# Kernel optimization log

Hardware: AMD Instinct MI355X
Metric: run time of the kernel (lower is better)

The kernel has to match this reference:

```python
import jax, jax.numpy as jnp
import numpy as np

EMBED = 1024
HEADS = 16
HEAD_DIM = EMBED // HEADS
FF = 4096
EPS = 1e-5


def layer_norm(x, g, b):
    mu = jnp.mean(x, axis=-1, keepdims=True)
    var = jnp.mean(jnp.square(x - mu), axis=-1, keepdims=True)
    return (x - mu) * jax.lax.rsqrt(var + EPS) * g + b


def setup_inputs() -> dict:
    key = jax.random.key(0)
    ks = jax.random.split(key, 16)
    s = 0.02
    x = jax.random.normal(ks[0], (4, 2048, EMBED), dtype=jnp.float32)
    d = {
        "x": x,
        "Wq": jax.random.normal(ks[1], (EMBED, EMBED), jnp.float32) * s,
        "bq": jnp.zeros((EMBED,), jnp.float32),
        "Wk": jax.random.normal(ks[2], (EMBED, EMBED), jnp.float32) * s,
        "bk": jnp.zeros((EMBED,), jnp.float32),
        "Wv": jax.random.normal(ks[3], (EMBED, EMBED), jnp.float32) * s,
        "bv": jnp.zeros((EMBED,), jnp.float32),
        "Wo": jax.random.normal(ks[4], (EMBED, EMBED), jnp.float32) * s,
        "bo": jnp.zeros((EMBED,), jnp.float32),
        "W1": jax.random.normal(ks[5], (EMBED, FF), jnp.float32) * s,
        "b1": jnp.zeros((FF,), jnp.float32),
        "W2": jax.random.normal(ks[6], (FF, EMBED), jnp.float32) * s,
        "b2": jnp.zeros((EMBED,), jnp.float32),
        "ln1_g": jnp.ones((EMBED,), jnp.float32),
        "ln1_b": jnp.zeros((EMBED,), jnp.float32),
        "ln2_g": jnp.ones((EMBED,), jnp.float32),
        "ln2_b": jnp.zeros((EMBED,), jnp.float32),
    }
    return d


def reference(x, Wq, bq, Wk, bk, Wv, bv, Wo, bo, W1, b1, W2, b2, ln1_g, ln1_b, ln2_g, ln2_b):
    B, S, E = x.shape
    scale = np.sqrt(HEAD_DIM).astype(np.float32)
    # project and split heads: (B, H, S, Dh)
    def heads(t):
        return t.reshape(B, S, HEADS, HEAD_DIM).transpose(0, 2, 1, 3)
    Q = heads(x @ Wq + bq)
    K = heads(x @ Wk + bk)
    V = heads(x @ Wv + bv)
    scores = jnp.einsum("bhqd,bhkd->bhqk", Q, K) / scale
    attn = jax.nn.softmax(scores, axis=-1)
    ctx = jnp.einsum("bhqk,bhkd->bhqd", attn, V)
    ctx = ctx.transpose(0, 2, 1, 3).reshape(B, S, E)
    attn_out = ctx @ Wo + bo
    x = layer_norm(x + attn_out, ln1_g, ln1_b)
    ff = jax.nn.relu(x @ W1 + b1) @ W2 + b2
    x = layer_norm(x + ff, ln2_g, ln2_b)
    return x
```

## Files before the change

kernel.cpp:

```cpp
#include <hip/hip_runtime.h>
#include <stdint.h>

typedef uint16_t u16;
typedef __bf16 bf16x8 __attribute__((ext_vector_type(8)));
typedef float f32x4 __attribute__((ext_vector_type(4)));

__device__ __forceinline__ float bf2f(u16 u) {
  union { uint32_t i; float f; } v; v.i = ((uint32_t)u) << 16; return v.f;
}
__device__ __forceinline__ u16 f2bf(float f) {
  union { float f; uint32_t i; } v; v.f = f;
  uint32_t r = v.i + 0x7fffu + ((v.i >> 16) & 1u);
  return (u16)(r >> 16);
}
__device__ __forceinline__ uint32_t pack2(float a, float b) {
  return (uint32_t)f2bf(a) | ((uint32_t)f2bf(b) << 16);
}
__device__ __forceinline__ void gll16(const u16* g, u16* l) {
  __builtin_amdgcn_global_load_lds((const __attribute__((address_space(1))) void*)g,
                                   (__attribute__((address_space(3))) void*)l, 16, 0, 0);
}

__global__ __launch_bounds__(256) void f32_to_bf16(
    const float* __restrict__ in, u16* __restrict__ out)
{
  int idx = blockIdx.x * 256 + threadIdx.x;
  float4 v = *(const float4*)(in + (size_t)idx * 4);
  uint2 o;
  o.x = pack2(v.x, v.y);
  o.y = pack2(v.z, v.w);
  *(uint2*)(out + (size_t)idx * 4) = o;
}

__global__ __launch_bounds__(256) void concat_bias(
    const float* __restrict__ a, const float* __restrict__ b,
    const float* __restrict__ c, float* __restrict__ o)
{
  int i = blockIdx.x * 256 + threadIdx.x;
  float v = (i < 1024) ? a[i] : ((i < 2048) ? b[i - 1024] : c[i - 2048]);
  o[i] = v;
}

__global__ __launch_bounds__(256) void transpose_f2b(
    const float* __restrict__ in, u16* __restrict__ out, int R, int C, int ldo)
{
  __shared__ u16 tile[32][33];
  int c0 = blockIdx.x * 32, r0 = blockIdx.y * 32;
  int x = threadIdx.x, y = threadIdx.y;
#pragma unroll
  for (int i = 0; i < 32; i += 8)
    tile[y + i][x] = f2bf(in[(size_t)(r0 + y + i) * C + (c0 + x)]);
  __syncthreads();
#pragma unroll
  for (int i = 0; i < 32; i += 8)
    out[(size_t)(c0 + y + i) * ldo + (r0 + x)] = tile[x][y + i];
}

__global__ __launch_bounds__(256) void transpose_v(
    const u16* __restrict__ src, u16* __restrict__ dst)
{
  __shared__ u16 tile[64][72];
  int kc = blockIdx.x;
  int bh = blockIdx.y;
  int b = bh >> 4, h = bh & 15;
  int t = threadIdx.x;
  int r = t >> 3;
  int c0 = (t & 7) * 8;
  const u16* s0 = src + ((size_t)(b * 2048 + kc * 64 + r) * 3072) + h * 64 + c0;
#pragma unroll
  for (int hh = 0; hh < 2; hh++)
    *(uint4*)(&tile[r + hh * 32][c0]) = *(const uint4*)(s0 + (size_t)hh * 32 * 3072);
  __syncthreads();
#pragma unroll
  for (int hh = 0; hh < 2; hh++) {
    int d = r + hh * 32;
    u16 vals[8];
#pragma unroll
    for (int p = 0; p < 8; p++) {
      int pos = c0 + p;
      int key = ((pos & 3) << 4) | ((pos >> 2) & 15);
      vals[p] = tile[key][d];
    }
    *(uint4*)(dst + ((size_t)bh * 64 + d) * 2048 + (size_t)kc * 64 + c0) = *(uint4*)vals;
  }
}

#define BM 128
#define BN 128
#define BK 32

__global__ __launch_bounds__(256, 2) void gemm_bt(
    const u16* __restrict__ A, const u16* __restrict__ BT,
    const float* __restrict__ bias, u16* __restrict__ C,
    int N, int K, int lda, int ldb, int ldc, int relu, int addC)
{
  __shared__ __align__(16) u16 As[BM][BK];
  __shared__ __align__(16) u16 Bs[BN][BK];
  int tid = threadIdx.x;
  int m0 = blockIdx.y * BM, n0 = blockIdx.x * BN;
  int wave = tid >> 6, lane = tid & 63;
  int quad = lane >> 4, tr = lane & 15;
  int wm = (wave >> 1) * 64, wn = (wave & 1) * 64;

  f32x4 zero = {0.f, 0.f, 0.f, 0.f};
  f32x4 acc[4][4];
#pragma unroll
  for (int i = 0; i < 4; i++)
#pragma unroll
    for (int j = 0; j < 4; j++) acc[i][j] = zero;

  int r_s = tid >> 2;
  int c_s = (tid & 3) * 8;
  const u16* Aptr = A + (size_t)(m0 + r_s) * lda + c_s;
  const u16* Bptr = BT + (size_t)(n0 + r_s) * ldb + c_s;
  u16* lA0 = &As[r_s][c_s];
  u16* lA1 = &As[r_s + 64][c_s];
  u16* lB0 = &Bs[r_s][c_s];
  u16* lB1 = &Bs[r_s + 64][c_s];

  for (int k0 = 0; k0 < K; k0 += BK) {
    gll16(Aptr + k0, lA0);
    gll16(Aptr + (size_t)64 * lda + k0, lA1);
    gll16(Bptr + k0, lB0);
    gll16(Bptr + (size_t)64 * ldb + k0, lB1);
    __syncthreads();
    bf16x8 af[4], bfr[4];
#pragma unroll
    for (int i = 0; i < 4; i++) af[i]  = *(const bf16x8*)(&As[wm + i*16 + tr][quad*8]);
#pragma unroll
    for (int j = 0; j < 4; j++) bfr[j] = *(const bf16x8*)(&Bs[wn + j*16 + tr][quad*8]);
#pragma unroll
    for (int i = 0; i < 4; i++)
#pragma unroll
      for (int j = 0; j < 4; j++)
        acc[i][j] = __builtin_amdgcn_mfma_f32_16x16x32_bf16(af[i], bfr[j], acc[i][j], 0, 0, 0);
    __syncthreads();
  }

#pragma unroll
  for (int j = 0; j < 4; j++) {
    int n = n0 + wn + j*16 + tr;
    float bv = bias ? bias[n] : 0.f;
#pragma unroll
    for (int i = 0; i < 4; i++) {
      int mrow = m0 + wm + i*16 + quad*4;
#pragma unroll
      for (int r = 0; r < 4; r++) {
        size_t idx = (size_t)(mrow + r) * ldc + n;
        float v = acc[i][j][r] + bv;
        if (addC) v += bf2f(C[idx]);
        if (relu) v = v > 0.f ? v : 0.f;
        C[idx] = f2bf(v);
      }
    }
  }
}

__global__ __launch_bounds__(512, 4) void flash_attn(
    const u16* __restrict__ Qb, const u16* __restrict__ Kb,
    const u16* __restrict__ Vtg, u16* __restrict__ Ob, int ldqkv, int ldo)
{
  __shared__ __align__(16) u16 Ks[64][72];
  __shared__ __align__(16) u16 Vt[64][72];
  __shared__ __align__(16) u16 Ps[8][32][72];

  const int S = 2048;
  int tid = threadIdx.x;
  int wv = tid >> 6, lane = tid & 63;
  int quad = lane >> 4, tr = lane & 15;
  int bh = blockIdx.y;
  int b = bh >> 4, h = bh & 15;
  int q0 = blockIdx.x * 256;
  int wq = wv * 32;
  size_t rowbase = (size_t)b * S;
  int colbase = h * 64;

  bf16x8 qf[2][2];
#pragma unroll
  for (int i = 0; i < 2; i++)
#pragma unroll
    for (int ks = 0; ks < 2; ks++)
      qf[i][ks] = *(const bf16x8*)(Qb + (rowbase + q0 + wq + i*16 + tr) * ldqkv
                                   + colbase + ks*32 + quad*8);

  f32x4 zero = {0.f, 0.f, 0.f, 0.f};
  f32x4 o[2][4];
  float lsum[2][4];
#pragma unroll
  for (int i = 0; i < 2; i++)
#pragma unroll
    for (int r = 0; r < 4; r++) lsum[i][r] = 0.f;
#pragma unroll
  for (int i = 0; i < 2; i++)
#pragma unroll
    for (int j = 0; j < 4; j++) o[i][j] = zero;

  const float sc = 0.125f;

  int srow = tid >> 3;
  int scol = (tid & 7) * 8;
  const u16* vt_base = Vtg + ((size_t)bh * 64 + srow) * 2048 + scol;

  for (int kv0 = 0; kv0 < S; kv0 += 64) {
    *(uint4*)(&Ks[srow][scol]) =
        *(const uint4*)(Kb + (rowbase + kv0 + srow) * ldqkv + colbase + scol);
    *(uint4*)(&Vt[srow][scol]) = *(const uint4*)(vt_base + kv0);
    __syncthreads();

    f32x4 s[2][4];
#pragma unroll
    for (int i = 0; i < 2; i++)
#pragma unroll
      for (int j = 0; j < 4; j++) s[i][j] = zero;
#pragma unroll
    for (int ks = 0; ks < 2; ks++) {
      bf16x8 kf[4];
#pragma unroll
      for (int j = 0; j < 4; j++)
        kf[j] = *(const bf16x8*)(&Ks[j*16 + tr][ks*32 + quad*8]);
#pragma unroll
      for (int i = 0; i < 2; i++)
#pragma unroll
        for (int j = 0; j < 4; j++)
          s[i][j] = __builtin_amdgcn_mfma_f32_16x16x32_bf16(qf[i][ks], kf[j], s[i][j], 0, 0, 0);
    }

#pragma unroll
    for (int i = 0; i < 2; i++) {
#pragma unroll
      for (int r = 0; r < 4; r++) {
        float p0 = __expf(s[i][0][r] * sc);
        float p1 = __expf(s[i][1][r] * sc);
        float p2 = __expf(s[i][2][r] * sc);
        float p3 = __expf(s[i][3][r] * sc);
        lsum[i][r] += (p0 + p1) + (p2 + p3);
        uint2 w;
        w.x = (__float_as_uint(p0) >> 16) | (__float_as_uint(p1) & 0xffff0000u);
        w.y = (__float_as_uint(p2) >> 16) | (__float_as_uint(p3) & 0xffff0000u);
        *(uint2*)(&Ps[wv][i*16 + quad*4 + r][tr*4]) = w;
      }
    }

#pragma unroll
    for (int ks = 0; ks < 2; ks++) {
      bf16x8 pf[2];
#pragma unroll
      for (int i = 0; i < 2; i++)
        pf[i] = *(const bf16x8*)(&Ps[wv][i*16 + tr][ks*32 + quad*8]);
#pragma unroll
      for (int jd = 0; jd < 4; jd++) {
        bf16x8 vf = *(const bf16x8*)(&Vt[jd*16 + tr][ks*32 + quad*8]);
#pragma unroll
        for (int i = 0; i < 2; i++)
          o[i][jd] = __builtin_amdgcn_mfma_f32_16x16x32_bf16(pf[i], vf, o[i][jd], 0, 0, 0);
      }
    }
    __syncthreads();
  }

#pragma unroll
  for (int i = 0; i < 2; i++) {
#pragma unroll
    for (int r = 0; r < 4; r++) {
      float l = lsum[i][r];
      l += __shfl_xor(l, 1, 64);
      l += __shfl_xor(l, 2, 64);
      l += __shfl_xor(l, 4, 64);
      l += __shfl_xor(l, 8, 64);
      float inv = 1.f / l;
      size_t qrow = rowbase + q0 + wq + i*16 + quad*4 + r;
#pragma unroll
      for (int jd = 0; jd < 4; jd++)
        Ob[qrow * ldo + colbase + jd*16 + tr] = f2bf(o[i][jd][r] * inv);
    }
  }
}

__global__ __launch_bounds__(256) void add_ln_a(
    const float* __restrict__ X, const u16* __restrict__ Rr,
    const float* __restrict__ G, const float* __restrict__ Bb,
    u16* __restrict__ Y)
{
  int row = blockIdx.x;
  int tid = threadIdx.x;
  __shared__ float sbuf[4], qbuf[4];
  float4 xv = *(const float4*)(X + (size_t)row * 1024 + tid * 4);
  uint2 ru = *(const uint2*)(Rr + (size_t)row * 1024 + tid * 4);
  const u16* rs = (const u16*)&ru;
  const float* xs = (const float*)&xv;
  float v[4];
  float s = 0.f, q = 0.f;
#pragma unroll
  for (int e = 0; e < 4; e++) {
    float a = xs[e] + bf2f(rs[e]);
    v[e] = a; s += a; q += a * a;
  }
#pragma unroll
  for (int off = 1; off < 64; off <<= 1) {
    s += __shfl_xor(s, off, 64);
    q += __shfl_xor(q, off, 64);
  }
  if ((tid & 63) == 0) { sbuf[tid >> 6] = s; qbuf[tid >> 6] = q; }
  __syncthreads();
  s = sbuf[0] + sbuf[1] + sbuf[2] + sbuf[3];
  q = qbuf[0] + qbuf[1] + qbuf[2] + qbuf[3];
  float mu  = s * (1.f / 1024.f);
  float var = q * (1.f / 1024.f) - mu * mu;
  float inv = rsqrtf(var + 1e-5f);
#pragma unroll
  for (int e = 0; e < 4; e++) {
    int col = tid * 4 + e;
    float yv = (v[e] - mu) * inv * G[col] + Bb[col];
    Y[(size_t)row * 1024 + col] = f2bf(yv);
  }
}

__global__ __launch_bounds__(256) void add_ln_b(
    const u16* __restrict__ X, const u16* __restrict__ Rr,
    const float* __restrict__ G, const float* __restrict__ Bb,
    float* __restrict__ Y)
{
  int row = blockIdx.x;
  int tid = threadIdx.x;
  __shared__ float sbuf[4], qbuf[4];
  uint2 xu = *(const uint2*)(X  + (size_t)row * 1024 + tid * 4);
  uint2 ru = *(const uint2*)(Rr + (size_t)row * 1024 + tid * 4);
  const u16* xs = (const u16*)&xu;
  const u16* rs = (const u16*)&ru;
  float v[4];
  float s = 0.f, q = 0.f;
#pragma unroll
  for (int e = 0; e < 4; e++) {
    float a = bf2f(xs[e]) + bf2f(rs[e]);
    v[e] = a; s += a; q += a * a;
  }
#pragma unroll
  for (int off = 1; off < 64; off <<= 1) {
    s += __shfl_xor(s, off, 64);
    q += __shfl_xor(q, off, 64);
  }
  if ((tid & 63) == 0) { sbuf[tid >> 6] = s; qbuf[tid >> 6] = q; }
  __syncthreads();
  s = sbuf[0] + sbuf[1] + sbuf[2] + sbuf[3];
  q = qbuf[0] + qbuf[1] + qbuf[2] + qbuf[3];
  float mu  = s * (1.f / 1024.f);
  float var = q * (1.f / 1024.f) - mu * mu;
  float inv = rsqrtf(var + 1e-5f);
  float4 yv;
  float* yp = (float*)&yv;
#pragma unroll
  for (int e = 0; e < 4; e++) {
    int col = tid * 4 + e;
    yp[e] = (v[e] - mu) * inv * G[col] + Bb[col];
  }
  *(float4*)(Y + (size_t)row * 1024 + tid * 4) = yv;
}

extern "C" void kernel_launch(void* const* d_in, const int* in_sizes, int n_in,
                              void* d_out, int out_size, void* d_ws, size_t ws_size,
                              hipStream_t stream) {
  const float* x   = (const float*)d_in[0];
  const float* Wq  = (const float*)d_in[1];
  const float* bq  = (const float*)d_in[2];
  const float* Wk  = (const float*)d_in[3];
  const float* bk  = (const float*)d_in[4];
  const float* Wv  = (const float*)d_in[5];
  const float* bv  = (const float*)d_in[6];
  const float* Wo  = (const float*)d_in[7];
  const float* bo  = (const float*)d_in[8];
  const float* W1  = (const float*)d_in[9];
  const float* b1  = (const float*)d_in[10];
  const float* W2  = (const float*)d_in[11];
  const float* b2  = (const float*)d_in[12];
  const float* g1  = (const float*)d_in[13];
  const float* be1 = (const float*)d_in[14];
  const float* g2  = (const float*)d_in[15];
  const float* be2 = (const float*)d_in[16];
  float* out = (float*)d_out;
  u16* ws  = (u16*)d_ws;

  const int Nrow = 8192, E = 1024, FFd = 4096;
  const size_t M1 = 1048576;
  u16* xb     = ws;
  u16* WqkvT  = ws + 8  * M1;
  u16* WoT    = ws + 11 * M1;
  u16* W1T    = ws + 12 * M1;
  u16* W2T    = ws + 16 * M1;
  u16* QKV    = ws + 20 * M1;
  u16* Vtg    = ws;
  u16* X1     = ws;
  u16* F2     = ws + 20 * M1;
  float* bqkv = (float*)d_out;
  u16*  AO    = (u16*)d_out;
  u16*  Hc    = (u16*)d_out;

  dim3 tb(256);
  dim3 tt(32, 8);
  f32_to_bf16<<<dim3(8192), tb, 0, stream>>>(x, xb);
  transpose_f2b<<<dim3(E/32,  E/32),  tt, 0, stream>>>(Wq, WqkvT,        E,   E,   E);
  transpose_f2b<<<dim3(E/32,  E/32),  tt, 0, stream>>>(Wk, WqkvT + 1*M1, E,   E,   E);
  transpose_f2b<<<dim3(E/32,  E/32),  tt, 0, stream>>>(Wv, WqkvT + 2*M1, E,   E,   E);
  transpose_f2b<<<dim3(E/32,  E/32),  tt, 0, stream>>>(Wo, WoT,          E,   E,   E);
  transpose_f2b<<<dim3(FFd/32,E/32),  tt, 0, stream>>>(W1, W1T,          E,   FFd, E);
  transpose_f2b<<<dim3(E/32,  FFd/32),tt, 0, stream>>>(W2, W2T,          FFd, E,   FFd);
  concat_bias<<<dim3(12), tb, 0, stream>>>(bq, bk, bv, bqkv);

  gemm_bt<<<dim3(24, Nrow/BM), tb, 0, stream>>>(xb, WqkvT, bqkv, QKV,
                                                3072, E, E, E, 3072, 0, 0);
  transpose_v<<<dim3(32, 64), tb, 0, stream>>>(QKV + 2048, Vtg);
  flash_attn<<<dim3(8, 64), dim3(512), 0, stream>>>(QKV, QKV + 1024, Vtg,
                                                    QKV + 2048, 3072, 3072);
  gemm_bt<<<dim3(8, Nrow/BM), tb, 0, stream>>>(QKV + 2048, WoT, bo, AO,
                                               E, E, 3072, E, E, 0, 0);
  add_ln_a<<<dim3(Nrow), tb, 0, stream>>>(x, AO, g1, be1, X1);

  for (int c = 0; c < 2; c++) {
    gemm_bt<<<dim3(16, Nrow/BM), tb, 0, stream>>>(
        X1, W1T + (size_t)c * 2048 * E, b1 + c * 2048, Hc,
        2048, E, E, E, 2048, 1, 0);
    gemm_bt<<<dim3(8, Nrow/BM), tb, 0, stream>>>(
        Hc, W2T + (size_t)c * 2048, (c == 0 ? b2 : (const float*)nullptr), F2,
        E, 2048, 2048, FFd, E, 0, (c == 0 ? 0 : 1));
  }

  add_ln_b<<<dim3(Nrow), tb, 0, stream>>>(X1, F2, g2, be2, out);
}
```

Measured before the change: 593.5 us.

## Double GEMM K-tile, add XOR-swizzled LDS layout, use direct-to-LDS loads in attention

```diff
diff --git a/kernel.cpp b/kernel.cpp
--- a/kernel.cpp
+++ b/kernel.cpp
@@ -87,7 +87,7 @@
 
 #define BM 128
 #define BN 128
-#define BK 32
+#define BK 64
 
 __global__ __launch_bounds__(256, 2) void gemm_bt(
     const u16* __restrict__ A, const u16* __restrict__ BT,
@@ -101,6 +101,7 @@
   int wave = tid >> 6, lane = tid & 63;
   int quad = lane >> 4, tr = lane & 15;
   int wm = (wave >> 1) * 64, wn = (wave & 1) * 64;
+  int tr7 = tr & 7;
 
   f32x4 zero = {0.f, 0.f, 0.f, 0.f};
   f32x4 acc[4][4];
@@ -109,31 +110,35 @@
 #pragma unroll
     for (int j = 0; j < 4; j++) acc[i][j] = zero;
 
-  int r_s = tid >> 2;
-  int c_s = (tid & 3) * 8;
-  const u16* Aptr = A + (size_t)(m0 + r_s) * lda + c_s;
-  const u16* Bptr = BT + (size_t)(n0 + r_s) * ldb + c_s;
-  u16* lA0 = &As[r_s][c_s];
-  u16* lA1 = &As[r_s + 64][c_s];
-  u16* lB0 = &Bs[r_s][c_s];
-  u16* lB1 = &Bs[r_s + 64][c_s];
+  int srow = tid >> 3;
+  int sblk = (tid & 7) ^ (srow & 7);
+  const u16* Abase = A  + (size_t)(m0 + srow) * lda + sblk * 8;
+  const u16* Bbase = BT + (size_t)(n0 + srow) * ldb + sblk * 8;
+  u16* la = &As[0][0] + tid * 8;
+  u16* lb = &Bs[0][0] + tid * 8;
 
   for (int k0 = 0; k0 < K; k0 += BK) {
-    gll16(Aptr + k0, lA0);
-    gll16(Aptr + (size_t)64 * lda + k0, lA1);
-    gll16(Bptr + k0, lB0);
-    gll16(Bptr + (size_t)64 * ldb + k0, lB1);
+#pragma unroll
+    for (int R = 0; R < 4; R++) {
+      gll16(Abase + (size_t)(R * 32) * lda + k0, la + R * 2048);
+      gll16(Bbase + (size_t)(R * 32) * ldb + k0, lb + R * 2048);
+    }
     __syncthreads();
-    bf16x8 af[4], bfr[4];
-#pragma unroll
-    for (int i = 0; i < 4; i++) af[i]  = *(const bf16x8*)(&As[wm + i*16 + tr][quad*8]);
-#pragma unroll
-    for (int j = 0; j < 4; j++) bfr[j] = *(const bf16x8*)(&Bs[wn + j*16 + tr][quad*8]);
-#pragma unroll
-    for (int i = 0; i < 4; i++)
+#pragma unroll
+    for (int ks = 0; ks < 2; ks++) {
+      bf16x8 af[4], bfr[4];
+#pragma unroll
+      for (int i = 0; i < 4; i++)
+        af[i]  = *(const bf16x8*)(&As[wm + i*16 + tr][(((ks*4 + quad) ^ tr7)) * 8]);
 #pragma unroll
       for (int j = 0; j < 4; j++)
-        acc[i][j] = __builtin_amdgcn_mfma_f32_16x16x32_bf16(af[i], bfr[j], acc[i][j], 0, 0, 0);
+        bfr[j] = *(const bf16x8*)(&Bs[wn + j*16 + tr][(((ks*4 + quad) ^ tr7)) * 8]);
+#pragma unroll
+      for (int i = 0; i < 4; i++)
+#pragma unroll
+        for (int j = 0; j < 4; j++)
+          acc[i][j] = __builtin_amdgcn_mfma_f32_16x16x32_bf16(af[i], bfr[j], acc[i][j], 0, 0, 0);
+    }
     __syncthreads();
   }
 
@@ -156,18 +161,19 @@
   }
 }
 
-__global__ __launch_bounds__(512, 4) void flash_attn(
+__global__ __launch_bounds__(512, 6) void flash_attn(
     const u16* __restrict__ Qb, const u16* __restrict__ Kb,
     const u16* __restrict__ Vtg, u16* __restrict__ Ob, int ldqkv, int ldo)
 {
-  __shared__ __align__(16) u16 Ks[64][72];
-  __shared__ __align__(16) u16 Vt[64][72];
+  __shared__ __align__(16) u16 Ks[64][64];
+  __shared__ __align__(16) u16 Vt[64][64];
   __shared__ __align__(16) u16 Ps[8][32][72];
 
   const int S = 2048;
   int tid = threadIdx.x;
   int wv = tid >> 6, lane = tid & 63;
   int quad = lane >> 4, tr = lane & 15;
+  int tr7 = tr & 7;
   int bh = blockIdx.y;
   int b = bh >> 4, h = bh & 15;
   int q0 = blockIdx.x * 256;
@@ -198,13 +204,15 @@
   const float sc = 0.125f;
 
   int srow = tid >> 3;
-  int scol = (tid & 7) * 8;
-  const u16* vt_base = Vtg + ((size_t)bh * 64 + srow) * 2048 + scol;
+  int sblk = (tid & 7) ^ (srow & 7);
+  const u16* kgbase = Kb + (rowbase + srow) * ldqkv + colbase + sblk * 8;
+  const u16* vgbase = Vtg + ((size_t)bh * 64 + srow) * 2048 + sblk * 8;
+  u16* kl = &Ks[0][0] + tid * 8;
+  u16* vl = &Vt[0][0] + tid * 8;
 
   for (int kv0 = 0; kv0 < S; kv0 += 64) {
-    *(uint4*)(&Ks[srow][scol]) =
-        *(const uint4*)(Kb + (rowbase + kv0 + srow) * ldqkv + colbase + scol);
-    *(uint4*)(&Vt[srow][scol]) = *(const uint4*)(vt_base + kv0);
+    gll16(kgbase + (size_t)kv0 * ldqkv, kl);
+    gll16(vgbase + kv0, vl);
     __syncthreads();
 
     f32x4 s[2][4];
@@ -217,7 +225,7 @@
       bf16x8 kf[4];
 #pragma unroll
       for (int j = 0; j < 4; j++)
-        kf[j] = *(const bf16x8*)(&Ks[j*16 + tr][ks*32 + quad*8]);
+        kf[j] = *(const bf16x8*)(&Ks[j*16 + tr][((ks*4 + quad) ^ tr7) * 8]);
 #pragma unroll
       for (int i = 0; i < 2; i++)
 #pragma unroll
@@ -249,7 +257,7 @@
         pf[i] = *(const bf16x8*)(&Ps[wv][i*16 + tr][ks*32 + quad*8]);
 #pragma unroll
       for (int jd = 0; jd < 4; jd++) {
-        bf16x8 vf = *(const bf16x8*)(&Vt[jd*16 + tr][ks*32 + quad*8]);
+        bf16x8 vf = *(const bf16x8*)(&Vt[jd*16 + tr][((ks*4 + quad) ^ tr7) * 8]);
 #pragma unroll
         for (int i = 0; i < 2; i++)
           o[i][jd] = __builtin_amdgcn_mfma_f32_16x16x32_bf16(pf[i], vf, o[i][jd], 0, 0, 0);
```

After: 865.5 us. +45.8%, slower.
